# Kernel optimization log

Hardware: AMD Instinct MI355X
Metric: run time of the kernel (lower is better)

Reference implementation:

```python
import jax, jax.numpy as jnp
import numpy as np

GRID_SIZE = 5
SPLINE_ORDER = 3
GRID_MIN, GRID_MAX = -1.0, 1.0
LN_EPS = 1e-5


def _make_grid():
    # Extended knot grid shared across input features: (grid_size + 2*order + 1,)
    h = (GRID_MAX - GRID_MIN) / GRID_SIZE
    return jnp.arange(-SPLINE_ORDER, GRID_SIZE + SPLINE_ORDER + 1, dtype=jnp.float32) * h + GRID_MIN


def b_splines(x, grid):
    # x: (B, in) -> bases: (B, in, grid_size + spline_order)
    xe = x[..., None]  # (B, in, 1)
    bases = ((xe >= grid[:-1]) & (xe < grid[1:])).astype(x.dtype)
    for k in range(1, SPLINE_ORDER + 1):
        left = (xe - grid[: -(k + 1)]) / (grid[k:-1] - grid[: -(k + 1)])
        right = (grid[k + 1:] - xe) / (grid[k + 1:] - grid[1:-k])
        bases = left * bases[..., :-1] + right * bases[..., 1:]
    return bases


def setup_inputs() -> dict:
    key = jax.random.key(0)
    ks = jax.random.split(key, 5)
    B, IN, OUT, COEF = 16384, 1024, 512, GRID_SIZE + SPLINE_ORDER
    return {
        "rgb_features": jax.random.normal(ks[0], (B, IN // 2), jnp.float32),
        "tactile_features": jax.random.normal(ks[1], (B, IN // 2), jnp.float32),
        "base_weight": jax.random.normal(ks[2], (OUT, IN), jnp.float32) * 0.02,
        "spline_weight": jax.random.normal(ks[3], (OUT, IN, COEF), jnp.float32) * 0.02,
        "spline_scaler": 1.0 + 0.02 * jax.random.normal(ks[4], (OUT, IN), jnp.float32),
        "ln_gamma": jnp.ones((OUT,), jnp.float32),
        "ln_beta": jnp.zeros((OUT,), jnp.float32),
    }


def reference(rgb_features, tactile_features, base_weight, spline_weight, spline_scaler, ln_gamma, ln_beta):
    x = jnp.concatenate((rgb_features, tactile_features), axis=1)  # (B, 1024)
    grid = _make_grid()
    # KANLinear: base path (SiLU + linear) + spline path (B-spline basis + linear)
    base_out = jnp.einsum("bi,oi->bo", jax.nn.silu(x), base_weight)
    bases = b_splines(x, grid)  # (B, in, coef)
    scaled_w = spline_weight * spline_scaler[..., None]  # (out, in, coef)
    spline_out = jnp.einsum("bik,oik->bo", bases, scaled_w)
    fused = base_out + spline_out
    # LayerNorm over last dim
    mu = jnp.mean(fused, axis=-1, keepdims=True)
    var = jnp.var(fused, axis=-1, keepdims=True)
    fused = (fused - mu) * jax.lax.rsqrt(var + LN_EPS) * ln_gamma + ln_beta
    # Dropout is identity in eval mode
    return fused
```

## Files before the change

### kernel.cpp

```cpp
#include <hip/hip_runtime.h>
#include <cstdint>
#include <cstddef>


#define BATCH    16384
#define OUT_DIM  512
#define KTOT     9216
#define BM       128
#define BK       64
#define NCHUNK        144
#define SPLINE_CHUNKS 128

typedef __attribute__((ext_vector_type(8))) short  short8;
typedef __attribute__((ext_vector_type(4))) float  f32x4;

static __device__ __forceinline__ unsigned short f2bf(float f) {
    unsigned int u = __float_as_uint(f);
    unsigned int r = u + 0x7fffu + ((u >> 16) & 1u);
    return (unsigned short)(r >> 16);
}

__global__ void prep_w_kernel(const float* __restrict__ bw,
                              const float* __restrict__ sw,
                              const float* __restrict__ sc,
                              unsigned short* __restrict__ Wp) {
    int t = blockIdx.x * 256 + threadIdx.x;
    int o = t / 1152;
    int g = t - o * 1152;
    int sz = o & 7;
    unsigned short o8[8];
    size_t dst;
    if (g < 1024) {
        float s = sc[(size_t)o * 1024 + g];
        const float* w = sw + ((size_t)o * 1024 + g) * 8;
        #pragma unroll
        for (int k = 0; k < 8; ++k) o8[k] = f2bf(w[k] * s);
        dst = (size_t)o * KTOT + (size_t)(g >> 3) * 64 + (size_t)(((g & 7) ^ sz)) * 8;
    } else {
        int gi = g - 1024;
        const float* w = bw + (size_t)o * 1024 + gi * 8;
        #pragma unroll
        for (int k = 0; k < 8; ++k) o8[k] = f2bf(w[k]);
        dst = (size_t)o * KTOT + (size_t)8192 + (size_t)(gi >> 3) * 64 + (size_t)(((gi & 7) ^ sz)) * 8;
    }
    *reinterpret_cast<short8*>(Wp + dst) = *reinterpret_cast<const short8*>(o8);
}

static __device__ __forceinline__ void basis8(float x, unsigned* out) {
    float tpos = (x + 2.2f) * 2.5f;
    float fj   = floorf(tpos);
    int   j    = (int)fj;
    float u  = tpos - fj;
    float v  = 1.f - u;
    float u2 = u * u;
    float u3 = u2 * u;
    const float c6 = 1.f / 6.f;
    float n0 = v * v * v * c6;
    float n3 = u3 * c6;
    float n1 = __builtin_fmaf(0.5f, u3, __builtin_fmaf(-1.f, u2, 4.f * c6));
    float n2 = 1.f - n0 - n1 - n3;
    unsigned p0, p1;
    asm("v_cvt_pk_bf16_f32 %0, %1, %2" : "=v"(p0) : "v"(n0), "v"(n1));
    asm("v_cvt_pk_bf16_f32 %0, %1, %2" : "=v"(p1) : "v"(n2), "v"(n3));
    int sh = (j << 4) - 48;
    int c  = sh & 16;
    int w  = (sh - c) >> 5;
    unsigned long long P = ((unsigned long long)p1 << 32) | p0;
    unsigned long long T = P << c;
    unsigned t0 = (unsigned)T;
    unsigned t1 = (unsigned)(T >> 32);
    unsigned t2 = c ? (p1 >> 16) : 0u;
    #pragma unroll
    for (int i = 0; i < 4; ++i) {
        unsigned r = 0u;
        r = (w == i    ) ? t0 : r;
        r = (w == i - 1) ? t1 : r;
        r = (w == i - 2) ? t2 : r;
        out[i] = r;
    }
}

template<bool SPLIT>
__launch_bounds__(1024, 4)
__global__ void kan_gemm_kernel(const float* __restrict__ rgb,
                                const float* __restrict__ tac,
                                const unsigned short* __restrict__ Wp,
                                float* __restrict__ dest_base) {
    __shared__ unsigned short At[2][BM][BK];
    __shared__ unsigned short Bt[2][OUT_DIM][BK];

    const int tid  = threadIdx.x;
    const int lane = tid & 63;
    const int wid  = tid >> 6;
    const int b0   = blockIdx.x * BM;
    const int wr   = wid & 1;
    const int wc   = wid >> 1;
    const int ksp  = SPLIT ? (int)blockIdx.y : 0;
    const int kc0  = SPLIT ? (ksp ? 72 : 0)             : 0;
    const int kcS  = SPLIT ? (ksp ? SPLINE_CHUNKS : 72) : SPLINE_CHUNKS;
    const int kc1  = SPLIT ? (ksp ? NCHUNK : 72)        : NCHUNK;
    float* dest = dest_base + (size_t)ksp * BATCH * OUT_DIM;

    const int ar  = tid >> 3;
    const int af_ = tid & 7;
    const bool rev = (((wid >> 2) ^ wid) & 1) != 0;

    f32x4 acc[4][4];
    #pragma unroll
    for (int m = 0; m < 4; ++m)
        #pragma unroll
        for (int n = 0; n < 4; ++n)
            acc[m][n] = (f32x4){0.f, 0.f, 0.f, 0.f};

    auto mfma_half = [&](int ab, int bb, int ks) {
        int cb = ks * 4 + (lane >> 4);
        short8 afr[4];
        #pragma unroll
        for (int m = 0; m < 4; ++m) {
            int row = wr * 64 + m * 16 + (lane & 15);
            afr[m] = *reinterpret_cast<const short8*>(&At[ab][row][(cb ^ (row & 7)) * 8]);
        }
        #pragma unroll
        for (int n = 0; n < 4; ++n) {
            int row = wc * 64 + n * 16 + (lane & 15);
            short8 bfr = *reinterpret_cast<const short8*>(
                &Bt[bb][row][(cb ^ (row & 7)) * 8]);
            #pragma unroll
            for (int m = 0; m < 4; ++m)
                acc[m][n] = __builtin_amdgcn_mfma_f32_16x16x32_bf16(
                    afr[m], bfr, acc[m][n], 0, 0, 0);
        }
    };

    auto mfma_step = [&](int ab, int bb) {
        if (rev) { mfma_half(ab, bb, 1); mfma_half(ab, bb, 0); }
        else     { mfma_half(ab, bb, 0); mfma_half(ab, bb, 1); }
    };

    auto loadx_s = [&](int c) -> float {
        int i0 = c * 8;
        const float* xs = (i0 < 512) ? rgb : tac;
        int ic = i0 & 511;
        return xs[(size_t)(b0 + ar) * 512 + ic + af_];
    };

    auto loadx_b = [&](int c, f32x4& xa, f32x4& xb) {
        int i0 = (c - SPLINE_CHUNKS) * 64;
        const float* xs = (i0 < 512) ? rgb : tac;
        int ic = i0 & 511;
        const float* xp = xs + (size_t)(b0 + ar) * 512 + ic + af_ * 8;
        xa = *reinterpret_cast<const f32x4*>(xp);
        xb = *reinterpret_cast<const f32x4*>(xp + 4);
    };

    auto silupack = [&](const f32x4& xa, const f32x4& xb, unsigned* o) {
        float s[8];
        #pragma unroll
        for (int q = 0; q < 4; ++q) {
            float a = xa[q];
            s[q]     = a * __builtin_amdgcn_rcpf(1.f + __expf(-a));
            float b = xb[q];
            s[q + 4] = b * __builtin_amdgcn_rcpf(1.f + __expf(-b));
        }
        #pragma unroll
        for (int q = 0; q < 4; ++q)
            asm("v_cvt_pk_bf16_f32 %0, %1, %2"
                : "=v"(o[q]) : "v"(s[2 * q]), "v"(s[2 * q + 1]));
    };

    auto writeA = [&](const unsigned* o4, int ab) {
        *reinterpret_cast<short8*>(&At[ab][ar][(af_ ^ (ar & 7)) * 8]) =
            *reinterpret_cast<const short8*>(o4);
    };

    auto gload_B = [&](int kc, int buf) {
        int k0g = kc * BK;
        #pragma unroll
        for (int rp = 0; rp < 4; ++rp) {
            int row0 = wid * 32 + rp * 8;
            const unsigned short* gp =
                Wp + (size_t)(row0 + (lane >> 3)) * KTOT + k0g + (lane & 7) * 8;
            __builtin_amdgcn_global_load_lds(
                (const __attribute__((address_space(1))) unsigned int*)gp,
                (__attribute__((address_space(3))) unsigned int*)&Bt[buf][row0][0],
                16, 0, 0);
        }
    };

    gload_B(kc0, 0);
    gload_B(kc0 + 1 < kc1 ? kc0 + 1 : kc1 - 1, 1);
    {
        float x0 = loadx_s(kc0);
        unsigned o4[4];
        basis8(x0, o4);
        writeA(o4, 0);
    }
    float xn = (kc0 + 1 < kcS) ? loadx_s(kc0 + 1) : 0.f;
    asm volatile("s_waitcnt vmcnt(4) lgkmcnt(0)" ::: "memory");
    __builtin_amdgcn_sched_barrier(0);
    __builtin_amdgcn_s_barrier();
    __builtin_amdgcn_sched_barrier(0);

    for (int t = kc0; t < kcS; ++t) {
        const int  buf   = (t - kc0) & 1;
        const bool moreA = (t + 1 < kcS);
        float xnn = (t + 2 < kcS) ? loadx_s(t + 2) : 0.f;
        unsigned o4[4];
        if (moreA) { basis8(xn, o4); writeA(o4, buf ^ 1); }
        mfma_step(buf, buf);
        xn = xnn;
        __builtin_amdgcn_sched_barrier(0);
        __builtin_amdgcn_s_barrier();
        __builtin_amdgcn_sched_barrier(0);
        int tn = (t + 2 < kc1) ? t + 2 : kc1 - 1;
        gload_B(tn, buf);
        asm volatile("s_waitcnt vmcnt(4) lgkmcnt(0)" ::: "memory");
        __builtin_amdgcn_sched_barrier(0);
        __builtin_amdgcn_s_barrier();
        __builtin_amdgcn_sched_barrier(0);
    }

    if (kcS < kc1) {
        f32x4 xa{}, xb{};
        {
            f32x4 a0, b0;
            loadx_b(kcS, a0, b0);
            unsigned o4[4];
            silupack(a0, b0, o4);
            writeA(o4, (kcS - kc0) & 1);
            if (kcS + 1 < kc1) loadx_b(kcS + 1, xa, xb);
            asm volatile("s_waitcnt lgkmcnt(0)" ::: "memory");
            __builtin_amdgcn_sched_barrier(0);
            __builtin_amdgcn_s_barrier();
            __builtin_amdgcn_sched_barrier(0);
        }
        for (int t = kcS; t < kc1; ++t) {
            const int  buf   = (t - kc0) & 1;
            const bool moreA = (t + 1 < kc1);
            const bool moreX = (t + 2 < kc1);
            f32x4 na, nb;
            if (moreX) loadx_b(t + 2, na, nb);
            unsigned o4[4];
            if (moreA) { silupack(xa, xb, o4); writeA(o4, buf ^ 1); }
            mfma_step(buf, buf);
            __builtin_amdgcn_sched_barrier(0);
            __builtin_amdgcn_s_barrier();
            __builtin_amdgcn_sched_barrier(0);
            int tn = moreX ? t + 2 : kc1 - 1;
            gload_B(tn, buf);
            asm volatile("s_waitcnt vmcnt(4) lgkmcnt(0)" ::: "memory");
            __builtin_amdgcn_sched_barrier(0);
            __builtin_amdgcn_s_barrier();
            __builtin_amdgcn_sched_barrier(0);
            if (moreX) { xa = na; xb = nb; }
        }
    }

    #pragma unroll
    for (int m = 0; m < 4; ++m) {
        int row = b0 + wr * 64 + m * 16 + ((lane >> 4) << 2);
        #pragma unroll
        for (int n = 0; n < 4; ++n) {
            int col = wc * 64 + n * 16 + (lane & 15);
            #pragma unroll
            for (int jj = 0; jj < 4; ++jj)
                dest[(size_t)(row + jj) * OUT_DIM + col] = acc[m][n][jj];
        }
    }
}

__global__ void reduce_ln_kernel(const float* __restrict__ P0,
                                 const float* __restrict__ P1,
                                 const float* __restrict__ gamma,
                                 const float* __restrict__ beta,
                                 float* __restrict__ out) {
    int row  = blockIdx.x * 4 + (threadIdx.x >> 6);
    int lane = threadIdx.x & 63;
    const float* p0 = P0 + (size_t)row * OUT_DIM;
    const float* p1 = P1 + (size_t)row * OUT_DIM;
    f32x4 a0 = *reinterpret_cast<const f32x4*>(p0 + lane * 4);
    f32x4 a1 = *reinterpret_cast<const f32x4*>(p0 + 256 + lane * 4);
    f32x4 b0 = *reinterpret_cast<const f32x4*>(p1 + lane * 4);
    f32x4 b1 = *reinterpret_cast<const f32x4*>(p1 + 256 + lane * 4);
    f32x4 v0, v1;
    #pragma unroll
    for (int q = 0; q < 4; ++q) { v0[q] = a0[q] + b0[q]; v1[q] = a1[q] + b1[q]; }
    float s = 0.f, ss = 0.f;
    #pragma unroll
    for (int q = 0; q < 4; ++q) {
        s  += v0[q] + v1[q];
        ss += v0[q] * v0[q] + v1[q] * v1[q];
    }
    #pragma unroll
    for (int off = 1; off < 64; off <<= 1) {
        s  += __shfl_xor(s, off);
        ss += __shfl_xor(ss, off);
    }
    float mu  = s * (1.f / 512.f);
    float var = ss * (1.f / 512.f) - mu * mu;
    float rs  = rsqrtf(var + 1e-5f);
    f32x4 g0 = *reinterpret_cast<const f32x4*>(gamma + lane * 4);
    f32x4 g1 = *reinterpret_cast<const f32x4*>(gamma + 256 + lane * 4);
    f32x4 e0 = *reinterpret_cast<const f32x4*>(beta + lane * 4);
    f32x4 e1 = *reinterpret_cast<const f32x4*>(beta + 256 + lane * 4);
    float* po = out + (size_t)row * OUT_DIM;
    f32x4 r0, r1;
    #pragma unroll
    for (int q = 0; q < 4; ++q) {
        r0[q] = (v0[q] - mu) * rs * g0[q] + e0[q];
        r1[q] = (v1[q] - mu) * rs * g1[q] + e1[q];
    }
    *reinterpret_cast<f32x4*>(po + lane * 4)       = r0;
    *reinterpret_cast<f32x4*>(po + 256 + lane * 4) = r1;
}

__global__ void ln_kernel(float* __restrict__ io,
                          const float* __restrict__ gamma,
                          const float* __restrict__ beta) {
    int row  = blockIdx.x * 4 + (threadIdx.x >> 6);
    int lane = threadIdx.x & 63;
    float* p = io + (size_t)row * OUT_DIM;
    f32x4 v0 = *reinterpret_cast<const f32x4*>(p + lane * 4);
    f32x4 v1 = *reinterpret_cast<const f32x4*>(p + 256 + lane * 4);
    float s = 0.f, ss = 0.f;
    #pragma unroll
    for (int q = 0; q < 4; ++q) {
        s  += v0[q] + v1[q];
        ss += v0[q] * v0[q] + v1[q] * v1[q];
    }
    #pragma unroll
    for (int off = 1; off < 64; off <<= 1) {
        s  += __shfl_xor(s, off);
        ss += __shfl_xor(ss, off);
    }
    float mu  = s * (1.f / 512.f);
    float var = ss * (1.f / 512.f) - mu * mu;
    float rs  = rsqrtf(var + 1e-5f);
    f32x4 g0 = *reinterpret_cast<const f32x4*>(gamma + lane * 4);
    f32x4 g1 = *reinterpret_cast<const f32x4*>(gamma + 256 + lane * 4);
    f32x4 e0 = *reinterpret_cast<const f32x4*>(beta + lane * 4);
    f32x4 e1 = *reinterpret_cast<const f32x4*>(beta + 256 + lane * 4);
    f32x4 r0, r1;
    #pragma unroll
    for (int q = 0; q < 4; ++q) {
        r0[q] = (v0[q] - mu) * rs * g0[q] + e0[q];
        r1[q] = (v1[q] - mu) * rs * g1[q] + e1[q];
    }
    *reinterpret_cast<f32x4*>(p + lane * 4)       = r0;
    *reinterpret_cast<f32x4*>(p + 256 + lane * 4) = r1;
}

extern "C" void kernel_launch(void* const* d_in, const int* in_sizes, int n_in,
                              void* d_out, int out_size, void* d_ws, size_t ws_size,
                              hipStream_t stream) {
    const float* rgb   = (const float*)d_in[0];
    const float* tac   = (const float*)d_in[1];
    const float* bw    = (const float*)d_in[2];
    const float* sw    = (const float*)d_in[3];
    const float* sc    = (const float*)d_in[4];
    const float* gamma = (const float*)d_in[5];
    const float* beta  = (const float*)d_in[6];
    float* out = (float*)d_out;
    unsigned short* Wp = (unsigned short*)d_ws;

    prep_w_kernel<<<2304, 256, 0, stream>>>(bw, sw, sc, Wp);

    const size_t PART = (size_t)BATCH * OUT_DIM * sizeof(float);
    const size_t POFF = 16ull << 20;
    if (ws_size >= POFF + 2 * PART) {
        float* P = (float*)((char*)d_ws + POFF);
        dim3 g(BATCH / BM, 2);
        kan_gemm_kernel<true><<<g, 1024, 0, stream>>>(rgb, tac, Wp, P);
        reduce_ln_kernel<<<BATCH / 4, 256, 0, stream>>>(
            P, P + (size_t)BATCH * OUT_DIM, gamma, beta, out);
    } else {
        dim3 g(BATCH / BM, 1);
        kan_gemm_kernel<false><<<g, 1024, 0, stream>>>(rgb, tac, Wp, out);
        ln_kernel<<<BATCH / 4, 256, 0, stream>>>(out, gamma, beta);
    }
}
```

Measured before the change: 191.0 us.

## Interleave LDS fragment reads with MFMA clusters and raise MFMA wave priority

Restructures the main loop so each K-step is split into two halves: fragments for one half are read from LDS and then an MFMA cluster runs under s_setprio(1) while the next global B load is issued. The A-tile write and the B-tile prefetch overlap with the second MFMA cluster, and vmcnt waits are loosened so more loads stay in flight. The per-wave reversed ordering is removed. The change adds more barriers per iteration and uses hand-tuned waitcnt values that must match the real number of outstanding loads.

```diff
diff --git a/kernel.cpp b/kernel.cpp
--- a/kernel.cpp
+++ b/kernel.cpp
@@ -103,7 +103,6 @@
 
     const int ar  = tid >> 3;
     const int af_ = tid & 7;
-    const bool rev = (((wid >> 2) ^ wid) & 1) != 0;
 
     f32x4 acc[4][4];
     #pragma unroll
@@ -112,9 +111,8 @@
         for (int n = 0; n < 4; ++n)
             acc[m][n] = (f32x4){0.f, 0.f, 0.f, 0.f};
 
-    auto mfma_half = [&](int ab, int bb, int ks) {
+    auto frag_read = [&](short8* afr, short8* bfr, int ab, int bb, int ks) {
         int cb = ks * 4 + (lane >> 4);
-        short8 afr[4];
         #pragma unroll
         for (int m = 0; m < 4; ++m) {
             int row = wr * 64 + m * 16 + (lane & 15);
@@ -123,18 +121,19 @@
         #pragma unroll
         for (int n = 0; n < 4; ++n) {
             int row = wc * 64 + n * 16 + (lane & 15);
-            short8 bfr = *reinterpret_cast<const short8*>(
-                &Bt[bb][row][(cb ^ (row & 7)) * 8]);
+            bfr[n] = *reinterpret_cast<const short8*>(&Bt[bb][row][(cb ^ (row & 7)) * 8]);
+        }
+    };
+
+    auto mfma_cluster = [&](const short8* afr, const short8* bfr) {
+        __builtin_amdgcn_s_setprio(1);
+        #pragma unroll
+        for (int n = 0; n < 4; ++n)
             #pragma unroll
             for (int m = 0; m < 4; ++m)
                 acc[m][n] = __builtin_amdgcn_mfma_f32_16x16x32_bf16(
-                    afr[m], bfr, acc[m][n], 0, 0, 0);
-        }
-    };
-
-    auto mfma_step = [&](int ab, int bb) {
-        if (rev) { mfma_half(ab, bb, 1); mfma_half(ab, bb, 0); }
-        else     { mfma_half(ab, bb, 0); mfma_half(ab, bb, 1); }
+                    afr[m], bfr[n], acc[m][n], 0, 0, 0);
+        __builtin_amdgcn_s_setprio(0);
     };
 
     auto loadx_s = [&](int c) -> float {
@@ -187,16 +186,16 @@
         }
     };
 
+    float x0 = loadx_s(kc0);
     gload_B(kc0, 0);
     gload_B(kc0 + 1 < kc1 ? kc0 + 1 : kc1 - 1, 1);
     {
-        float x0 = loadx_s(kc0);
         unsigned o4[4];
         basis8(x0, o4);
         writeA(o4, 0);
     }
     float xn = (kc0 + 1 < kcS) ? loadx_s(kc0 + 1) : 0.f;
-    asm volatile("s_waitcnt vmcnt(4) lgkmcnt(0)" ::: "memory");
+    asm volatile("s_waitcnt vmcnt(0) lgkmcnt(0)" ::: "memory");
     __builtin_amdgcn_sched_barrier(0);
     __builtin_amdgcn_s_barrier();
     __builtin_amdgcn_sched_barrier(0);
@@ -204,20 +203,31 @@
     for (int t = kc0; t < kcS; ++t) {
         const int  buf   = (t - kc0) & 1;
         const bool moreA = (t + 1 < kcS);
+        short8 afr[4], bfr[4];
+        frag_read(afr, bfr, buf, buf, 0);
         float xnn = (t + 2 < kcS) ? loadx_s(t + 2) : 0.f;
         unsigned o4[4];
-        if (moreA) { basis8(xn, o4); writeA(o4, buf ^ 1); }
-        mfma_step(buf, buf);
-        xn = xnn;
-        __builtin_amdgcn_sched_barrier(0);
+        if (moreA) basis8(xn, o4);
         __builtin_amdgcn_s_barrier();
-        __builtin_amdgcn_sched_barrier(0);
+        asm volatile("s_waitcnt lgkmcnt(0)" ::: "memory");
+        __builtin_amdgcn_sched_barrier(0);
+        mfma_cluster(afr, bfr);
+        __builtin_amdgcn_sched_barrier(0);
+        __builtin_amdgcn_s_barrier();
+        frag_read(afr, bfr, buf, buf, 1);
+        if (moreA) writeA(o4, buf ^ 1);
+        asm volatile("s_waitcnt lgkmcnt(0)" ::: "memory");
+        __builtin_amdgcn_sched_barrier(0);
+        __builtin_amdgcn_s_barrier();
         int tn = (t + 2 < kc1) ? t + 2 : kc1 - 1;
         gload_B(tn, buf);
-        asm volatile("s_waitcnt vmcnt(4) lgkmcnt(0)" ::: "memory");
+        __builtin_amdgcn_sched_barrier(0);
+        mfma_cluster(afr, bfr);
+        asm volatile("s_waitcnt vmcnt(5)" ::: "memory");
         __builtin_amdgcn_sched_barrier(0);
         __builtin_amdgcn_s_barrier();
         __builtin_amdgcn_sched_barrier(0);
+        xn = xnn;
     }
 
     if (kcS < kc1) {
@@ -238,17 +248,28 @@
             const int  buf   = (t - kc0) & 1;
             const bool moreA = (t + 1 < kc1);
             const bool moreX = (t + 2 < kc1);
+            short8 afr[4], bfr[4];
+            frag_read(afr, bfr, buf, buf, 0);
             f32x4 na, nb;
             if (moreX) loadx_b(t + 2, na, nb);
             unsigned o4[4];
-            if (moreA) { silupack(xa, xb, o4); writeA(o4, buf ^ 1); }
-            mfma_step(buf, buf);
-            __builtin_amdgcn_sched_barrier(0);
+            if (moreA) silupack(xa, xb, o4);
             __builtin_amdgcn_s_barrier();
-            __builtin_amdgcn_sched_barrier(0);
+            asm volatile("s_waitcnt lgkmcnt(0)" ::: "memory");
+            __builtin_amdgcn_sched_barrier(0);
+            mfma_cluster(afr, bfr);
+            __builtin_amdgcn_sched_barrier(0);
+            __builtin_amdgcn_s_barrier();
+            frag_read(afr, bfr, buf, buf, 1);
+            if (moreA) writeA(o4, buf ^ 1);
+            asm volatile("s_waitcnt lgkmcnt(0)" ::: "memory");
+            __builtin_amdgcn_sched_barrier(0);
+            __builtin_amdgcn_s_barrier();
             int tn = moreX ? t + 2 : kc1 - 1;
             gload_B(tn, buf);
-            asm volatile("s_waitcnt vmcnt(4) lgkmcnt(0)" ::: "memory");
+            __builtin_amdgcn_sched_barrier(0);
+            mfma_cluster(afr, bfr);
+            asm volatile("s_waitcnt vmcnt(6)" ::: "memory");
             __builtin_amdgcn_sched_barrier(0);
             __builtin_amdgcn_s_barrier();
             __builtin_amdgcn_sched_barrier(0);
```

Result: slower. 205.3 us (+7.5%).
